# Kernel optimization log

Measured on AMD Instinct MI355X. Metric: run time of the kernel, lower is better.

## Reference

```python
import jax, jax.numpy as jnp
import numpy as np

B, A, NC, DIR, LMAX, MAXZ, NORB = 8, 64, 128, 4, 2, 10, 14
NF = NC * DIR * (2 * LMAX + 1)   # 2560
O2 = NORB * NORB                 # 196
AO = A * NORB                    # 896
LOG2 = float(np.log(2.0))

def ssp(v):  # spk shifted softplus
    return jax.nn.softplus(v) - LOG2

def setup_inputs():
    key = jax.random.key(0)
    ks = jax.random.split(key, 12)
    Z = jax.random.randint(ks[0], (B, A), 1, MAXZ)
    idx = np.arange(A)
    nbh_np = np.stack([np.delete(idx, i) for i in range(A)], 0)  # [A, A-1]: all atoms except self
    nbh = jnp.asarray(np.broadcast_to(nbh_np[None], (B, A, A - 1)).copy(), dtype=jnp.int32)
    x = jax.random.normal(ks[1], (B, A, NC), jnp.float32)
    Vijkl = jax.random.normal(ks[2], (B, A, A - 1, NF), jnp.float32) * 0.1
    sc = 1.0 / np.sqrt(NF)
    W_off = jax.random.normal(ks[3], (NF, O2), jnp.float32) * sc
    b_off = jnp.zeros((O2,), jnp.float32)
    W_on = jax.random.normal(ks[4], (NF, O2), jnp.float32) * sc
    b_on = jnp.zeros((O2,), jnp.float32)
    W_ovoff = jax.random.normal(ks[5], (NF, O2), jnp.float32) * sc
    b_ovoff = jnp.zeros((O2,), jnp.float32)
    ov_emb = jax.random.normal(ks[6], (MAXZ, O2), jnp.float32) * 0.1  # trainable overlap onsite embedding
    orb_energies = jax.random.normal(ks[7], (MAXZ, NORB), jnp.float32)  # h0 energies
    s0_energies = jnp.ones((MAXZ, NORB), jnp.float32)                   # s0 init = ones
    W1 = jax.random.normal(ks[8], (NC, NC // 2), jnp.float32) / np.sqrt(NC)
    b1 = jnp.zeros((NC // 2,), jnp.float32)
    W2 = jax.random.normal(ks[9], (NC // 2, 1), jnp.float32) / np.sqrt(NC // 2)
    b2 = jnp.zeros((1,), jnp.float32)
    return {"Z": Z, "nbh": nbh, "x": x, "Vijkl": Vijkl,
            "W_off": W_off, "b_off": b_off, "W_on": W_on, "b_on": b_on,
            "W_ovoff": W_ovoff, "b_ovoff": b_ovoff, "ov_emb": ov_emb,
            "orb_energies": orb_energies, "s0_energies": s0_energies,
            "W1": W1, "b1": b1, "W2": W2, "b2": b2}

def reference(Z, nbh, x, Vijkl, W_off, b_off, W_on, b_on, W_ovoff, b_ovoff,
              ov_emb, orb_energies, s0_energies, W1, b1, W2, b2):
    # permutation that reorders neighbor slots (plus appended zero/self slot) into atom order
    ar = jnp.broadcast_to(jnp.arange(A, dtype=nbh.dtype)[None, :, None], (B, A, 1))
    sort_idx = jnp.argsort(jnp.concatenate([nbh, ar], axis=2), axis=2)  # [B,A,A]
    eyeA = jnp.eye(A, dtype=Vijkl.dtype)
    eyeAO = jnp.eye(AO, dtype=Vijkl.dtype)

    def assemble(off, on):
        # off: [B,A,A-1,O2] pair blocks; on: [B,A,O2] onsite blocks
        offz = jnp.concatenate([off, jnp.zeros((B, A, 1, O2), off.dtype)], axis=2)  # zero self block at slot A-1
        offg = jnp.take_along_axis(offz, sort_idx[..., None], axis=2)               # [B,A,A,O2]
        M = offg + eyeA[None, :, :, None] * on[:, :, None, :]
        M = M.reshape(B, A, A, NORB, NORB).transpose(0, 1, 3, 2, 4).reshape(B, AO, AO)
        return 0.5 * (M + M.transpose(0, 2, 1))

    # Hamiltonian: offsite Dense + onsite Dense mean-aggregated over pairs
    H_off = Vijkl @ W_off + b_off                       # [B,A,A-1,O2]
    H_on = jnp.mean(Vijkl @ W_on + b_on, axis=2)        # [B,A,O2]
    H = assemble(H_off, H_on)
    # h0 single-atom diagonal (orb mask is all-active -> full diagonal)
    H = H + eyeAO[None] * orb_energies[Z].reshape(B, 1, AO)

    # Overlap: offsite Dense + onsite embedding lookup
    S_off = Vijkl @ W_ovoff + b_ovoff
    S_on = ov_emb[Z]                                    # [B,A,O2]
    S = assemble(S_off, S_on)
    S = S + eyeAO[None] * s0_energies[Z].reshape(B, 1, AO)

    # energy head: Dense->ssp->Dense->ScaleShift(0,1), sum over atoms
    Ei = ssp(x @ W1 + b1) @ W2 + b2                     # [B,A,1]
    E = jnp.sum(Ei, axis=1)                             # [B,1]
    return H, S, E
```

## Files before the change

kernel.cpp:

```cpp
#include <hip/hip_runtime.h>

#define B_      8
#define A_      64
#define NPAIR   63
#define NC_     128
#define NF_     2560
#define O2_     196
#define NORB_   14
#define AO_     896
#define NCOLS   588
#define CSTRIDE 640
#define KSTEPS  80
#define BM      64
#define BN      640
#define BSTEP_BYTES 40960

typedef short bf16x8 __attribute__((ext_vector_type(8)));
typedef float f32x4  __attribute__((ext_vector_type(4)));

__device__ __forceinline__ unsigned f2bf(float f) {
    unsigned u = __builtin_bit_cast(unsigned, f);
    return (u + 0x7fffu + ((u >> 16) & 1u)) >> 16;
}

__global__ __launch_bounds__(512)
void prep_energy(const float* __restrict__ W_off, const float* __restrict__ W_ovoff,
                 const float* __restrict__ W_on, unsigned short* __restrict__ Bws,
                 const float* __restrict__ x, const float* __restrict__ W1,
                 const float* __restrict__ b1, const float* __restrict__ W2,
                 const float* __restrict__ b2, float* __restrict__ E) {
    const int t = threadIdx.x;
    if (blockIdx.x < KSTEPS) {
        __shared__ float wt[32 * BN];
        const int ks = blockIdx.x;
        for (int e = t; e < 32 * BN; e += 512) {
            int kl = e / BN, c = e - kl * BN;
            int kg = ks * 32 + kl;
            float v = 0.f;
            if (c < O2_)          v = W_off  [(size_t)kg * O2_ + c];
            else if (c < 2 * O2_) v = W_ovoff[(size_t)kg * O2_ + (c - O2_)];
            else if (c < 3 * O2_) v = W_on   [(size_t)kg * O2_ + (c - 2 * O2_)];
            wt[kl * BN + c] = v;
        }
        __syncthreads();
        unsigned short* out = Bws + (size_t)ks * (BN * 32);
        for (int e = t; e < BN * 4; e += 512) {
            int n = e >> 2, sg = e & 3;
            uint4 w;
            w.x = f2bf(wt[(sg * 8 + 0) * BN + n]) | (f2bf(wt[(sg * 8 + 1) * BN + n]) << 16);
            w.y = f2bf(wt[(sg * 8 + 2) * BN + n]) | (f2bf(wt[(sg * 8 + 3) * BN + n]) << 16);
            w.z = f2bf(wt[(sg * 8 + 4) * BN + n]) | (f2bf(wt[(sg * 8 + 5) * BN + n]) << 16);
            w.w = f2bf(wt[(sg * 8 + 6) * BN + n]) | (f2bf(wt[(sg * 8 + 7) * BN + n]) << 16);
            *(uint4*)(out + (size_t)n * 32 + sg * 8) = w;
        }
    } else {
        __shared__ float partial[8];
        const int b = blockIdx.x - KSTEPS;
        const int lane = t & 63;
        const int w = t >> 6;
        float esum = 0.f;
        for (int aa = 0; aa < 8; ++aa) {
            const int a = w * 8 + aa;
            const float* xr = x + (size_t)(b * A_ + a) * NC_;
            float hj = b1[lane];
            for (int k = 0; k < NC_; ++k) hj = fmaf(xr[k], W1[k * 64 + lane], hj);
            float sp = fmaxf(hj, 0.f) + log1pf(expf(-fabsf(hj))) - 0.69314718055994531f;
            float v = sp * W2[lane];
            for (int off = 32; off; off >>= 1) v += __shfl_down(v, off);
            if (lane == 0) esum += v + b2[0];
        }
        if (lane == 0) partial[w] = esum;
        __syncthreads();
        if (t == 0) {
            float e = 0.f;
            for (int k = 0; k < 8; ++k) e += partial[k];
            E[b] = e;
        }
    }
}

__global__ __launch_bounds__(512, 4)
void gemm_off(const float* __restrict__ V, const unsigned short* __restrict__ Bws,
              const float* __restrict__ b_off, const float* __restrict__ b_ovoff,
              const float* __restrict__ b_on, float* __restrict__ HSoff) {
    __shared__ alignas(16) float          Af32[2][BM * 32];
    __shared__ alignas(16) unsigned short Ab16[2][BM * 32];

    const int tid  = threadIdx.x;
    int mtb = blockIdx.x;
    mtb = (mtb & 7) * 63 + (mtb >> 3);
    const int mt   = mtb;
    const int lane = tid & 63;
    const int wv   = tid >> 6;
    const int wvu  = __builtin_amdgcn_readfirstlane(wv);

    const float* asrc = V + (size_t)(mt * BM + (tid >> 3)) * NF_ + (tid & 7) * 4;

    const char* bp = (const char*)Bws + (size_t)(wv * 80 + (lane & 15)) * 64 + (lane >> 4) * 16;
#define BFRAG(t_, nf_) (*(const bf16x8*)(bp + (size_t)(t_) * BSTEP_BYTES + (nf_) * 1024))

    f32x4 acc[4][5];
#pragma unroll
    for (int mf = 0; mf < 4; ++mf)
#pragma unroll
        for (int nf = 0; nf < 5; ++nf)
            acc[mf][nf] = (f32x4){0.f, 0.f, 0.f, 0.f};

    auto stage = [&](int buf, int t) {
        __builtin_amdgcn_global_load_lds(
            (const __attribute__((address_space(1))) void*)(asrc + (size_t)t * 32),
            (__attribute__((address_space(3))) void*)(&Af32[buf][wvu * 256]), 16, 0, 0);
    };

    const int crr = tid >> 3, cq = tid & 7;
    const int csl = ((cq >> 1) + ((crr + (crr >> 2)) & 3)) & 3;
    char* const cdst_base0 = (char*)&Ab16[0][0] + crr * 64 + csl * 16 + (cq & 1) * 8;
    char* const cdst_base1 = (char*)&Ab16[1][0] + crr * 64 + csl * 16 + (cq & 1) * 8;

    const unsigned klo4 = (unsigned)(lane >> 4);

#define AFRAG(abf_, mf_, Bb16_) {                                                   \
    const unsigned R_ = (unsigned)(lane & 15) + (mf_) * 16;                         \
    const unsigned sl_ = (klo4 + ((R_ + (R_ >> 2)) & 3)) & 3;                       \
    abf_ = *(const bf16x8*)((const char*)(Bb16_) + R_ * 64 + sl_ * 16); }

#define MFMA1(abf_, bq_, mf_, nf_) \
    acc[mf_][nf_] = __builtin_amdgcn_mfma_f32_16x16x32_bf16(abf_, bq_, acc[mf_][nf_], 0, 0, 0);

    bf16x8 bq0, bq1, bq2, bq3, bq4, abf;

    stage(0, 0);
    bq0 = BFRAG(0, 0); bq1 = BFRAG(0, 1); bq2 = BFRAG(0, 2); bq3 = BFRAG(0, 3); bq4 = BFRAG(0, 4);

    for (int t = 0; t < KSTEPS; ++t) {
        const int buf = t & 1;
        asm volatile("s_waitcnt vmcnt(5)" ::: "memory");
        __builtin_amdgcn_sched_barrier(0);
        __builtin_amdgcn_s_barrier();
        __builtin_amdgcn_sched_barrier(0);
        if (t + 1 < KSTEPS) stage(buf ^ 1, t + 1);

        {
            float4 cf = *(const float4*)((const char*)&Af32[buf][0] + tid * 16);
            unsigned lo, hi;
            asm("v_cvt_pk_bf16_f32 %0, %1, %2" : "=v"(lo) : "v"(cf.x), "v"(cf.y));
            asm("v_cvt_pk_bf16_f32 %0, %1, %2" : "=v"(hi) : "v"(cf.z), "v"(cf.w));
            uint2 cw = {lo, hi};
            *(uint2*)(buf ? cdst_base1 : cdst_base0) = cw;
        }
        asm volatile("s_waitcnt lgkmcnt(0)" ::: "memory");
        __builtin_amdgcn_sched_barrier(0);
        __builtin_amdgcn_s_barrier();
        __builtin_amdgcn_sched_barrier(0);

        const unsigned short* At = &Ab16[buf][0];
        AFRAG(abf, 0, At);
        __builtin_amdgcn_s_setprio(1);
        MFMA1(abf, bq0, 0, 0); MFMA1(abf, bq1, 0, 1); MFMA1(abf, bq2, 0, 2);
        MFMA1(abf, bq3, 0, 3); MFMA1(abf, bq4, 0, 4);
        __builtin_amdgcn_s_setprio(0);
        AFRAG(abf, 1, At);
        __builtin_amdgcn_s_setprio(1);
        MFMA1(abf, bq0, 1, 0); MFMA1(abf, bq1, 1, 1); MFMA1(abf, bq2, 1, 2);
        MFMA1(abf, bq3, 1, 3); MFMA1(abf, bq4, 1, 4);
        __builtin_amdgcn_s_setprio(0);
        AFRAG(abf, 2, At);
        __builtin_amdgcn_s_setprio(1);
        MFMA1(abf, bq0, 2, 0); MFMA1(abf, bq1, 2, 1); MFMA1(abf, bq2, 2, 2);
        MFMA1(abf, bq3, 2, 3); MFMA1(abf, bq4, 2, 4);
        __builtin_amdgcn_s_setprio(0);
        AFRAG(abf, 3, At);
        __builtin_amdgcn_s_setprio(1);
        MFMA1(abf, bq0, 3, 0); bq0 = BFRAG(t + 1, 0);
        MFMA1(abf, bq1, 3, 1); bq1 = BFRAG(t + 1, 1);
        MFMA1(abf, bq2, 3, 2); bq2 = BFRAG(t + 1, 2);
        MFMA1(abf, bq3, 3, 3); bq3 = BFRAG(t + 1, 3);
        MFMA1(abf, bq4, 3, 4); bq4 = BFRAG(t + 1, 4);
        __builtin_amdgcn_s_setprio(0);
        __builtin_amdgcn_sched_barrier(0);
    }

    const int c16 = lane & 15, rg = lane >> 4;
#pragma unroll
    for (int nf = 0; nf < 5; ++nf) {
        int C = wv * 80 + nf * 16 + c16;
        if (C >= NCOLS) continue;
        float bias = (C < O2_) ? b_off[C] : (C < 2 * O2_) ? b_ovoff[C - O2_] : b_on[C - 2 * O2_];
#pragma unroll
        for (int mf = 0; mf < 4; ++mf) {
            int R = mt * BM + mf * 16 + rg * 4;
            float* o = HSoff + (size_t)R * CSTRIDE + C;
            o[0]           = acc[mf][nf][0] + bias;
            o[CSTRIDE]     = acc[mf][nf][1] + bias;
            o[2 * CSTRIDE] = acc[mf][nf][2] + bias;
            o[3 * CSTRIDE] = acc[mf][nf][3] + bias;
        }
    }
#undef BFRAG
#undef AFRAG
#undef MFMA1
}

__global__ void hon_reduce(const float* __restrict__ HSoff, float* __restrict__ Hon) {
    const int g = blockIdx.x;
    const int t = threadIdx.x;
    if (t >= O2_) return;
    const float* p0 = HSoff + (size_t)g * NPAIR * CSTRIDE + 2 * O2_ + t;
    const float* p1 = p0 + (size_t)21 * CSTRIDE;
    const float* p2 = p0 + (size_t)42 * CSTRIDE;
    float a0 = 0.f, a1 = 0.f, a2 = 0.f;
#pragma unroll 3
    for (int j = 0; j < 21; ++j) {
        a0 += p0[0]; a1 += p1[0]; a2 += p2[0];
        p0 += CSTRIDE; p1 += CSTRIDE; p2 += CSTRIDE;
    }
    Hon[(size_t)g * O2_ + t] = (a0 + a1 + a2) * (1.f / (float)NPAIR);
}

__global__ __launch_bounds__(256)
void assemble_k(const float* __restrict__ HSoff, const float* __restrict__ Hon,
                const int* __restrict__ Z, const float* __restrict__ ov_emb,
                const float* __restrict__ orbE, const float* __restrict__ s0E,
                float* __restrict__ H, float* __restrict__ S) {
    __shared__ float Ai[NPAIR * 197];
    __shared__ float Bj[2][16 * 200];
    __shared__ float Dg[O2_];
    __shared__ float Dd[NORB_];

    const int bid = blockIdx.x;
    const int h = bid & 1, i = (bid >> 1) & 63, b = bid >> 7;
    const int t = threadIdx.x;
    const int g = b * A_ + i;
    const int z = Z[g];
    float* out = (h ? S : H) + (size_t)b * AO_ * AO_;

    const float* abase = HSoff + (size_t)g * NPAIR * CSTRIDE + h * O2_;
    for (int u = t; u < NPAIR * O2_; u += 256) {
        int jj = u / O2_, e = u - jj * O2_;
        Ai[jj * 197 + e] = abase[(size_t)jj * CSTRIDE + e];
    }
    if (t < O2_)   Dg[t] = h ? ov_emb[(size_t)z * O2_ + t]   : Hon[(size_t)g * O2_ + t];
    if (t < NORB_) Dd[t] = h ? s0E[(size_t)z * NORB_ + t]    : orbE[(size_t)z * NORB_ + t];

    auto stageB = [&](int buf, int jc) {
        for (int u = t; u < 16 * O2_; u += 256) {
            int jl = u / O2_, e = u - jl * O2_;
            int j = jc * 16 + jl;
            if (j != i) {
                int idx = (i < j) ? i : i - 1;
                Bj[buf][jl * 200 + e] =
                    HSoff[((size_t)(b * A_ + j) * NPAIR + idx) * CSTRIDE + h * O2_ + e];
            }
        }
    };
    stageB(0, 0);
    __syncthreads();

    const int tj = t / NORB_, tq = t - tj * NORB_;
    for (int jc = 0; jc < 4; ++jc) {
        if (jc < 3) stageB((jc + 1) & 1, jc + 1);
        if (t < 224) {
            const int j = jc * 16 + tj;
            const int cur = jc & 1;
#pragma unroll
            for (int p = 0; p < NORB_; ++p) {
                float v;
                if (j == i) {
                    v = 0.5f * (Dg[p * NORB_ + tq] + Dg[tq * NORB_ + p]);
                    if (p == tq) v += Dd[p];
                } else {
                    int jj = (j < i) ? j : j - 1;
                    v = 0.5f * (Ai[jj * 197 + p * NORB_ + tq] + Bj[cur][tj * 200 + tq * NORB_ + p]);
                }
                out[(size_t)(i * NORB_ + p) * AO_ + jc * 224 + t] = v;
            }
        }
        __syncthreads();
    }
}

extern "C" void kernel_launch(void* const* d_in, const int* in_sizes, int n_in,
                              void* d_out, int out_size, void* d_ws, size_t ws_size,
                              hipStream_t stream) {
    const int*   Z       = (const int*)  d_in[0];
    const float* x       = (const float*)d_in[2];
    const float* V       = (const float*)d_in[3];
    const float* W_off   = (const float*)d_in[4];
    const float* b_off   = (const float*)d_in[5];
    const float* W_on    = (const float*)d_in[6];
    const float* b_on    = (const float*)d_in[7];
    const float* W_ovoff = (const float*)d_in[8];
    const float* b_ovoff = (const float*)d_in[9];
    const float* ov_emb  = (const float*)d_in[10];
    const float* orbE    = (const float*)d_in[11];
    const float* s0E     = (const float*)d_in[12];
    const float* W1      = (const float*)d_in[13];
    const float* b1      = (const float*)d_in[14];
    const float* W2      = (const float*)d_in[15];
    const float* b2      = (const float*)d_in[16];

    float* H = (float*)d_out;
    float* S = H + (size_t)B_ * AO_ * AO_;
    float* E = S + (size_t)B_ * AO_ * AO_;

    char* ws = (char*)d_ws;
    unsigned short* Bws = (unsigned short*)ws;
    float* HSoff = (float*)(ws + (size_t)4  * 1024 * 1024);
    float* Hon   = (float*)(ws + (size_t)88 * 1024 * 1024);

    prep_energy<<<KSTEPS + B_, 512, 0, stream>>>(W_off, W_ovoff, W_on, Bws,
                                                 x, W1, b1, W2, b2, E);
    gemm_off   <<<504,  512, 0, stream>>>(V, Bws, b_off, b_ovoff, b_on, HSoff);
    hon_reduce <<<512,  256, 0, stream>>>(HSoff, Hon);
    assemble_k <<<1024, 256, 0, stream>>>(HSoff, Hon, Z, ov_emb, orbE, s0E, H, S);
}
```

Baseline: 263.7 us.

## Double GEMM M-tile to 128 rows with 1024-thread blocks and prefetch pipeline

The GEMM block now covers 128 rows using 16 waves arranged as 2 M-groups by 8 N-groups, so each B fragment load serves twice as many rows. The main loop is restructured to stage A two steps ahead and to do the fp32-to-bf16 conversion of the next tile between the two MFMA halves, leaving one barrier per step instead of two. The block-index swizzle is removed and the grid shrinks to 252 blocks, fewer than the number of CUs, so some CUs may sit idle. The 1024-thread blocks also raise register pressure.

```diff
diff --git a/kernel.cpp b/kernel.cpp
--- a/kernel.cpp
+++ b/kernel.cpp
@@ -11,7 +11,7 @@
 #define NCOLS   588
 #define CSTRIDE 640
 #define KSTEPS  80
-#define BM      64
+#define BM      128
 #define BN      640
 #define BSTEP_BYTES 40960
 
@@ -79,7 +79,7 @@
     }
 }
 
-__global__ __launch_bounds__(512, 4)
+__global__ __launch_bounds__(1024, 4)
 void gemm_off(const float* __restrict__ V, const unsigned short* __restrict__ Bws,
               const float* __restrict__ b_off, const float* __restrict__ b_ovoff,
               const float* __restrict__ b_on, float* __restrict__ HSoff) {
@@ -87,16 +87,15 @@
     __shared__ alignas(16) unsigned short Ab16[2][BM * 32];
 
     const int tid  = threadIdx.x;
-    int mtb = blockIdx.x;
-    mtb = (mtb & 7) * 63 + (mtb >> 3);
-    const int mt   = mtb;
+    const int mt   = blockIdx.x;
     const int lane = tid & 63;
     const int wv   = tid >> 6;
+    const int wm   = wv >> 3, wn = wv & 7;
     const int wvu  = __builtin_amdgcn_readfirstlane(wv);
 
     const float* asrc = V + (size_t)(mt * BM + (tid >> 3)) * NF_ + (tid & 7) * 4;
 
-    const char* bp = (const char*)Bws + (size_t)(wv * 80 + (lane & 15)) * 64 + (lane >> 4) * 16;
+    const char* bp = (const char*)Bws + (size_t)(wn * 80 + (lane & 15)) * 64 + (lane >> 4) * 16;
 #define BFRAG(t_, nf_) (*(const bf16x8*)(bp + (size_t)(t_) * BSTEP_BYTES + (nf_) * 1024))
 
     f32x4 acc[4][5];
@@ -114,81 +113,84 @@
 
     const int crr = tid >> 3, cq = tid & 7;
     const int csl = ((cq >> 1) + ((crr + (crr >> 2)) & 3)) & 3;
-    char* const cdst_base0 = (char*)&Ab16[0][0] + crr * 64 + csl * 16 + (cq & 1) * 8;
-    char* const cdst_base1 = (char*)&Ab16[1][0] + crr * 64 + csl * 16 + (cq & 1) * 8;
+    const unsigned cdst = (unsigned)(crr * 64 + csl * 16 + (cq & 1) * 8);
 
     const unsigned klo4 = (unsigned)(lane >> 4);
 
 #define AFRAG(abf_, mf_, Bb16_) {                                                   \
-    const unsigned R_ = (unsigned)(lane & 15) + (mf_) * 16;                         \
+    const unsigned R_ = (unsigned)(wm * 64 + (lane & 15) + (mf_) * 16);             \
     const unsigned sl_ = (klo4 + ((R_ + (R_ >> 2)) & 3)) & 3;                       \
     abf_ = *(const bf16x8*)((const char*)(Bb16_) + R_ * 64 + sl_ * 16); }
 
 #define MFMA1(abf_, bq_, mf_, nf_) \
     acc[mf_][nf_] = __builtin_amdgcn_mfma_f32_16x16x32_bf16(abf_, bq_, acc[mf_][nf_], 0, 0, 0);
 
-    bf16x8 bq0, bq1, bq2, bq3, bq4, abf;
+    bf16x8 bq0, bq1, bq2, bq3, bq4, af0, af1, af2, af3;
 
     stage(0, 0);
+    stage(1, 1);
     bq0 = BFRAG(0, 0); bq1 = BFRAG(0, 1); bq2 = BFRAG(0, 2); bq3 = BFRAG(0, 3); bq4 = BFRAG(0, 4);
+    asm volatile("s_waitcnt vmcnt(6)" ::: "memory");
+    {
+        float4 cf = *(const float4*)((const char*)&Af32[0][0] + tid * 16);
+        unsigned lo, hi;
+        asm("v_cvt_pk_bf16_f32 %0, %1, %2" : "=v"(lo) : "v"(cf.x), "v"(cf.y));
+        asm("v_cvt_pk_bf16_f32 %0, %1, %2" : "=v"(hi) : "v"(cf.z), "v"(cf.w));
+        uint2 cw = {lo, hi};
+        *(uint2*)((char*)&Ab16[0][0] + cdst) = cw;
+    }
+    asm volatile("s_waitcnt lgkmcnt(0)" ::: "memory");
+    __builtin_amdgcn_s_barrier();
+    __builtin_amdgcn_sched_barrier(0);
 
     for (int t = 0; t < KSTEPS; ++t) {
         const int buf = t & 1;
-        asm volatile("s_waitcnt vmcnt(5)" ::: "memory");
-        __builtin_amdgcn_sched_barrier(0);
-        __builtin_amdgcn_s_barrier();
-        __builtin_amdgcn_sched_barrier(0);
-        if (t + 1 < KSTEPS) stage(buf ^ 1, t + 1);
-
-        {
-            float4 cf = *(const float4*)((const char*)&Af32[buf][0] + tid * 16);
+        if (t + 2 < KSTEPS) stage(buf, t + 2);
+
+        AFRAG(af0, 0, &Ab16[buf][0]);
+        AFRAG(af1, 1, &Ab16[buf][0]);
+        __builtin_amdgcn_s_setprio(1);
+        MFMA1(af0, bq0, 0, 0); MFMA1(af0, bq1, 0, 1); MFMA1(af0, bq2, 0, 2);
+        MFMA1(af0, bq3, 0, 3); MFMA1(af0, bq4, 0, 4);
+        MFMA1(af1, bq0, 1, 0); MFMA1(af1, bq1, 1, 1); MFMA1(af1, bq2, 1, 2);
+        MFMA1(af1, bq3, 1, 3); MFMA1(af1, bq4, 1, 4);
+        __builtin_amdgcn_s_setprio(0);
+
+        if (t + 1 < KSTEPS) {
+            asm volatile("s_waitcnt vmcnt(5)" ::: "memory");
+            float4 cf = *(const float4*)((const char*)&Af32[buf ^ 1][0] + tid * 16);
             unsigned lo, hi;
             asm("v_cvt_pk_bf16_f32 %0, %1, %2" : "=v"(lo) : "v"(cf.x), "v"(cf.y));
             asm("v_cvt_pk_bf16_f32 %0, %1, %2" : "=v"(hi) : "v"(cf.z), "v"(cf.w));
             uint2 cw = {lo, hi};
-            *(uint2*)(buf ? cdst_base1 : cdst_base0) = cw;
-        }
+            *(uint2*)((char*)&Ab16[buf ^ 1][0] + cdst) = cw;
+        }
+
+        AFRAG(af2, 2, &Ab16[buf][0]);
+        AFRAG(af3, 3, &Ab16[buf][0]);
+        __builtin_amdgcn_s_setprio(1);
+        MFMA1(af2, bq0, 2, 0); MFMA1(af3, bq0, 3, 0); bq0 = BFRAG(t + 1, 0);
+        MFMA1(af2, bq1, 2, 1); MFMA1(af3, bq1, 3, 1); bq1 = BFRAG(t + 1, 1);
+        MFMA1(af2, bq2, 2, 2); MFMA1(af3, bq2, 3, 2); bq2 = BFRAG(t + 1, 2);
+        MFMA1(af2, bq3, 2, 3); MFMA1(af3, bq3, 3, 3); bq3 = BFRAG(t + 1, 3);
+        MFMA1(af2, bq4, 2, 4); MFMA1(af3, bq4, 3, 4); bq4 = BFRAG(t + 1, 4);
+        __builtin_amdgcn_s_setprio(0);
+
         asm volatile("s_waitcnt lgkmcnt(0)" ::: "memory");
         __builtin_amdgcn_sched_barrier(0);
         __builtin_amdgcn_s_barrier();
         __builtin_amdgcn_sched_barrier(0);
-
-        const unsigned short* At = &Ab16[buf][0];
-        AFRAG(abf, 0, At);
-        __builtin_amdgcn_s_setprio(1);
-        MFMA1(abf, bq0, 0, 0); MFMA1(abf, bq1, 0, 1); MFMA1(abf, bq2, 0, 2);
-        MFMA1(abf, bq3, 0, 3); MFMA1(abf, bq4, 0, 4);
-        __builtin_amdgcn_s_setprio(0);
-        AFRAG(abf, 1, At);
-        __builtin_amdgcn_s_setprio(1);
-        MFMA1(abf, bq0, 1, 0); MFMA1(abf, bq1, 1, 1); MFMA1(abf, bq2, 1, 2);
-        MFMA1(abf, bq3, 1, 3); MFMA1(abf, bq4, 1, 4);
-        __builtin_amdgcn_s_setprio(0);
-        AFRAG(abf, 2, At);
-        __builtin_amdgcn_s_setprio(1);
-        MFMA1(abf, bq0, 2, 0); MFMA1(abf, bq1, 2, 1); MFMA1(abf, bq2, 2, 2);
-        MFMA1(abf, bq3, 2, 3); MFMA1(abf, bq4, 2, 4);
-        __builtin_amdgcn_s_setprio(0);
-        AFRAG(abf, 3, At);
-        __builtin_amdgcn_s_setprio(1);
-        MFMA1(abf, bq0, 3, 0); bq0 = BFRAG(t + 1, 0);
-        MFMA1(abf, bq1, 3, 1); bq1 = BFRAG(t + 1, 1);
-        MFMA1(abf, bq2, 3, 2); bq2 = BFRAG(t + 1, 2);
-        MFMA1(abf, bq3, 3, 3); bq3 = BFRAG(t + 1, 3);
-        MFMA1(abf, bq4, 3, 4); bq4 = BFRAG(t + 1, 4);
-        __builtin_amdgcn_s_setprio(0);
-        __builtin_amdgcn_sched_barrier(0);
     }
 
     const int c16 = lane & 15, rg = lane >> 4;
 #pragma unroll
     for (int nf = 0; nf < 5; ++nf) {
-        int C = wv * 80 + nf * 16 + c16;
+        int C = wn * 80 + nf * 16 + c16;
         if (C >= NCOLS) continue;
         float bias = (C < O2_) ? b_off[C] : (C < 2 * O2_) ? b_ovoff[C - O2_] : b_on[C - 2 * O2_];
 #pragma unroll
         for (int mf = 0; mf < 4; ++mf) {
-            int R = mt * BM + mf * 16 + rg * 4;
+            int R = mt * BM + wm * 64 + mf * 16 + rg * 4;
             float* o = HSoff + (size_t)R * CSTRIDE + C;
             o[0]           = acc[mf][nf][0] + bias;
             o[CSTRIDE]     = acc[mf][nf][1] + bias;
@@ -310,7 +312,7 @@
 
     prep_energy<<<KSTEPS + B_, 512, 0, stream>>>(W_off, W_ovoff, W_on, Bws,
                                                  x, W1, b1, W2, b2, E);
-    gemm_off   <<<504,  512, 0, stream>>>(V, Bws, b_off, b_ovoff, b_on, HSoff);
-    hon_reduce <<<512,  256, 0, stream>>>(HSoff, Hon);
-    assemble_k <<<1024, 256, 0, stream>>>(HSoff, Hon, Z, ov_emb, orbE, s0E, H, S);
-}
+    gemm_off   <<<252,  1024, 0, stream>>>(V, Bws, b_off, b_ovoff, b_on, HSoff);
+    hon_reduce <<<512,  256,  0, stream>>>(HSoff, Hon);
+    assemble_k <<<1024, 256,  0, stream>>>(HSoff, Hon, Z, ov_emb, orbE, s0E, H, S);
+}
```

New measurement: 269.4 us. 1.02x slower.
